# Performance work log

Hardware: AMD Instinct MI355X
Metric: run time of the kernel (lower is better)

Reference implementation:

```python
import jax, jax.numpy as jnp
import numpy as np

# Tree / encoder dims (see shape_source): root + 4 middle + 16 leaves
T_DATA = 100000
T_V = 100
WIN = 2 * T_V - 1          # (T_V-1)*2 + 1 = 199, first MLP in_dim
HID = 256                  # hid_dim
N_MID = 4                  # numel(in_idx_list[0])  (middle-level latents)
N_LEAF = 16                # numel(out_idx_list[-1]) (leaf-level latents)


def setup_inputs() -> dict:
    key = jax.random.key(0)
    ks = jax.random.split(key, 6)
    sc = lambda k, shape, fan: jax.random.normal(k, shape, jnp.float32) * (1.0 / np.sqrt(fan))
    return {
        "V_in": jax.random.normal(ks[0], (T_DATA,), jnp.float32),
        "W1": sc(ks[1], (WIN, HID), WIN),
        "b1": jnp.zeros((HID,), jnp.float32),
        "W2": sc(ks[2], (HID, N_MID), HID),
        "b2": jnp.zeros((N_MID,), jnp.float32),
        # leaf_encoder = MLP(HID, HID, N_LEAF)
        "Wl1": sc(ks[3], (HID, HID), HID),
        "bl1": jnp.zeros((HID,), jnp.float32),
        "Wl2": sc(ks[4], (HID, N_LEAF), HID),
        "bl2": jnp.zeros((N_LEAF,), jnp.float32),
    }


def reference(V_in, W1, b1, W2, b2, Wl1, bl1, Wl2, bl2):
    """Vectorized LVAE_shGLM.Encoder: the original loops over every timestep t,
    slicing pad_V_in[t:t+2*T_V-1] and running MLP.encode chains per step.
    Here all T windows are processed as one batched GEMM chain.
    MLP.encode(x) = (h = relu(x@W1+b1), mu = h@W2+b2)."""
    T = V_in.shape[0]
    pad = jnp.zeros((T + 2 * (T_V - 1),), V_in.dtype).at[T_V - 1:T_V - 1 + T].set(V_in)
    idx = jnp.arange(T)[:, None] + jnp.arange(WIN)[None, :]
    windows = pad[idx]
    # middle encoder (level 0 of the dendritic tree)
    h_mid = jax.nn.relu(windows @ W1 + b1)          # [T, HID]
    mu_mid = h_mid @ W2 + b2                        # [T, N_MID]
    # leaf encoder consumes the middle hidden state
    h_leaf = jax.nn.relu(h_mid @ Wl1 + bl1)         # [T, HID]
    mu_leaf = h_leaf @ Wl2 + bl2                    # [T, N_LEAF]
    # up_mu_array[t] = [middle mus (count 0..N_MID), leaf mus (N_MID..sub_no-1)]
    return jnp.concatenate([mu_mid, mu_leaf], axis=1)  # [T, sub_no-1] = [T, 20]
```

## Files before the change

### kernel.cpp

```cpp
#include <hip/hip_runtime.h>


typedef __bf16 bf16;
typedef __bf16 bf16x8 __attribute__((ext_vector_type(8)));
typedef __bf16 bf16x4 __attribute__((ext_vector_type(4)));
typedef float  f32x4  __attribute__((ext_vector_type(4)));
typedef float  f32x16 __attribute__((ext_vector_type(16)));

constexpr int T_DATA = 100000;
constexpr int T_V    = 100;
constexpr int WIN    = 199;
constexpr int HID    = 256;
constexpr int BT     = 128;
constexpr int CSTR   = 264;
constexpr int VLEN   = 352;
constexpr int VSTR   = 360;

constexpr int PWL1_OFF = 104 * 512;
constexpr int PW2_OFF  = 232 * 512;
constexpr int PWL2_OFF = 240 * 512;

__global__ void pack_weights(const float* __restrict__ W1, const float* __restrict__ W2,
                             const float* __restrict__ Wl1, const float* __restrict__ Wl2,
                             bf16* __restrict__ ws) {
  const int gid  = blockIdx.x * blockDim.x + threadIdx.x;
  const int lane = gid & 63;
  const int grp  = gid >> 6;
  bf16x8 v;
  if (grp < 104) {
    const int kt = grp >> 3, nt = grp & 7, n = nt * 32 + (lane & 31);
#pragma unroll
    for (int j = 0; j < 8; ++j) {
      const int k = kt * 16 + (lane >> 5) * 8 + j;
      v[j] = (k < WIN) ? (bf16)W1[k * HID + n] : (bf16)0.0f;
    }
  } else if (grp < 232) {
    const int q = grp - 104;
    const int kt = q >> 3, nt = q & 7, n = nt * 32 + (lane & 31);
#pragma unroll
    for (int j = 0; j < 8; ++j) {
      const int k = kt * 16 + (lane >> 5) * 8 + j;
      v[j] = (bf16)Wl1[k * HID + n];
    }
  } else if (grp < 240) {
    const int kt = grp - 232, m = lane & 15;
#pragma unroll
    for (int j = 0; j < 8; ++j) {
      const int k = kt * 32 + (lane >> 4) * 8 + j;
      v[j] = (m < 4) ? (bf16)W2[k * 4 + m] : (bf16)0.0f;
    }
  } else {
    const int kt = grp - 240, m = lane & 15;
#pragma unroll
    for (int j = 0; j < 8; ++j) {
      const int k = kt * 32 + (lane >> 4) * 8 + j;
      v[j] = (bf16)Wl2[k * 16 + m];
    }
  }
  *reinterpret_cast<bf16x8*>(ws + (size_t)gid * 8) = v;
}

__global__ __launch_bounds__(512, 4) void fused_enc(
    const float* __restrict__ V, const float* __restrict__ b1,
    const float* __restrict__ b2, const float* __restrict__ bl1,
    const float* __restrict__ bl2, const bf16* __restrict__ ws,
    float* __restrict__ out) {
  __shared__ bf16 Vdup[8][VSTR];
  __shared__ bf16 hbuf[BT * CSTR];

  const int tid  = threadIdx.x;
  const int lane = tid & 63;
  const int w    = tid >> 6;
  const int c5   = lane & 31;
  const int hi   = lane >> 5;
  const int m    = lane & 15;
  const int g    = lane >> 4;
  const long t0  = (long)blockIdx.x * BT;

  for (int c = tid; c < 8 * VLEN; c += 512) {
    const int p = c / VLEN, q = c - p * VLEN;
    const long src = t0 + q + p - (T_V - 1);
    const float v = (src >= 0 && src < T_DATA) ? V[src] : 0.0f;
    Vdup[p][q] = (bf16)v;
  }
  __syncthreads();

  const int p  = lane & 7;
  const int qb = (c5 + hi * 8) - p;
  const bf16* vrow = &Vdup[p][0];

  f32x16 acc[4];
#pragma unroll
  for (int nt = 0; nt < 4; ++nt) acc[nt] = (f32x16){};

#pragma unroll
  for (int kt = 0; kt < 13; ++kt) {
    const bf16x8 a = *reinterpret_cast<const bf16x8*>(
        ws + (size_t)(kt * 8 + w) * 512 + lane * 8);
#pragma unroll
    for (int nt = 0; nt < 4; ++nt) {
      const bf16x8 b = *reinterpret_cast<const bf16x8*>(vrow + qb + nt * 32 + kt * 16);
      acc[nt] = __builtin_amdgcn_mfma_f32_32x32x16_bf16(a, b, acc[nt], 0, 0, 0);
    }
  }

  {
    f32x4 bb[4];
#pragma unroll
    for (int q = 0; q < 4; ++q)
      bb[q] = *reinterpret_cast<const f32x4*>(&b1[w * 32 + 8 * q + 4 * hi]);
#pragma unroll
    for (int nt = 0; nt < 4; ++nt) {
      const int t = nt * 32 + c5;
#pragma unroll
      for (int q = 0; q < 4; ++q) {
        bf16x4 hv;
#pragma unroll
        for (int i = 0; i < 4; ++i)
          hv[i] = (bf16)fmaxf(acc[nt][4 * q + i] + bb[q][i], 0.0f);
        *reinterpret_cast<bf16x4*>(&hbuf[t * CSTR + w * 32 + 8 * q + 4 * hi]) = hv;
      }
    }
  }
  __syncthreads();

#pragma unroll
  for (int nt = 0; nt < 4; ++nt) acc[nt] = (f32x16){};
#pragma unroll
  for (int kt = 0; kt < 16; ++kt) {
    const bf16x8 a = *reinterpret_cast<const bf16x8*>(
        ws + PWL1_OFF + (size_t)(kt * 8 + w) * 512 + lane * 8);
    const int koff = kt * 16 + hi * 8;
#pragma unroll
    for (int nt = 0; nt < 4; ++nt) {
      const bf16x8 b = *reinterpret_cast<const bf16x8*>(
          &hbuf[(nt * 32 + c5) * CSTR + koff]);
      acc[nt] = __builtin_amdgcn_mfma_f32_32x32x16_bf16(a, b, acc[nt], 0, 0, 0);
    }
  }

  f32x4 mu = {0.f, 0.f, 0.f, 0.f};
#pragma unroll
  for (int kt = 0; kt < 8; ++kt) {
    const bf16x8 a = *reinterpret_cast<const bf16x8*>(
        ws + PW2_OFF + (size_t)kt * 512 + lane * 8);
    const bf16x8 b = *reinterpret_cast<const bf16x8*>(
        &hbuf[(w * 16 + m) * CSTR + kt * 32 + g * 8]);
    mu = __builtin_amdgcn_mfma_f32_16x16x32_bf16(a, b, mu, 0, 0, 0);
  }
  {
    const long t = t0 + w * 16 + m;
    if (g == 0 && t < T_DATA) {
      const f32x4 b2v = *reinterpret_cast<const f32x4*>(b2);
      f32x4 o;
#pragma unroll
      for (int j = 0; j < 4; ++j) o[j] = mu[j] + b2v[j];
      *reinterpret_cast<f32x4*>(&out[t * 20]) = o;
    }
  }
  __syncthreads();

  {
    f32x4 bb[4];
#pragma unroll
    for (int q = 0; q < 4; ++q)
      bb[q] = *reinterpret_cast<const f32x4*>(&bl1[w * 32 + 8 * q + 4 * hi]);
#pragma unroll
    for (int nt = 0; nt < 4; ++nt) {
      const int t = nt * 32 + c5;
#pragma unroll
      for (int q = 0; q < 4; ++q) {
        bf16x4 hv;
#pragma unroll
        for (int i = 0; i < 4; ++i)
          hv[i] = (bf16)fmaxf(acc[nt][4 * q + i] + bb[q][i], 0.0f);
        *reinterpret_cast<bf16x4*>(&hbuf[t * CSTR + w * 32 + 8 * q + 4 * hi]) = hv;
      }
    }
  }
  __syncthreads();

  mu = (f32x4){0.f, 0.f, 0.f, 0.f};
#pragma unroll
  for (int kq = 0; kq < 8; ++kq) {
    const bf16x8 a = *reinterpret_cast<const bf16x8*>(
        ws + PWL2_OFF + (size_t)kq * 512 + lane * 8);
    const bf16x8 b = *reinterpret_cast<const bf16x8*>(
        &hbuf[(w * 16 + m) * CSTR + kq * 32 + g * 8]);
    mu = __builtin_amdgcn_mfma_f32_16x16x32_bf16(a, b, mu, 0, 0, 0);
  }
  {
    const long t = t0 + w * 16 + m;
    if (t < T_DATA) {
      const f32x4 blv = *reinterpret_cast<const f32x4*>(&bl2[g * 4]);
      f32x4 o;
#pragma unroll
      for (int j = 0; j < 4; ++j) o[j] = mu[j] + blv[j];
      *reinterpret_cast<f32x4*>(&out[t * 20 + 4 + g * 4]) = o;
    }
  }
}

extern "C" void kernel_launch(void* const* d_in, const int* in_sizes, int n_in,
                              void* d_out, int out_size, void* d_ws, size_t ws_size,
                              hipStream_t stream) {
  const float* V   = (const float*)d_in[0];
  const float* W1  = (const float*)d_in[1];
  const float* b1  = (const float*)d_in[2];
  const float* W2  = (const float*)d_in[3];
  const float* b2  = (const float*)d_in[4];
  const float* Wl1 = (const float*)d_in[5];
  const float* bl1 = (const float*)d_in[6];
  const float* Wl2 = (const float*)d_in[7];
  const float* bl2 = (const float*)d_in[8];
  bf16* ws = (bf16*)d_ws;
  float* out = (float*)d_out;

  pack_weights<<<62, 256, 0, stream>>>(W1, W2, Wl1, Wl2, ws);

  const int grid = (T_DATA + BT - 1) / BT;
  fused_enc<<<grid, 512, 0, stream>>>(V, b1, b2, bl1, bl2, ws, out);
}
```

Before: 40.21 us.

## Split token tile into two halves and software-pipeline the MLP stages

The 128-timestep block is split into two 64-row halves with separate LDS hidden buffers. The second half's first-layer GEMM is interleaved with the first half's leaf GEMM, and the small output GEMMs are divided across warps 0-3 and 4-7 so they run concurrently. The aim is to keep the matrix cores busy across stage boundaries and shrink the per-stage accumulator footprint. The cost is extra barriers, duplicated bias loads and more complex control flow. The LDS footprint stays about the same.

```diff
diff --git a/kernel.cpp b/kernel.cpp
--- a/kernel.cpp
+++ b/kernel.cpp
@@ -66,7 +66,8 @@
     const float* __restrict__ bl2, const bf16* __restrict__ ws,
     float* __restrict__ out) {
   __shared__ bf16 Vdup[8][VSTR];
-  __shared__ bf16 hbuf[BT * CSTR];
+  __shared__ bf16 hbufA[64 * CSTR];
+  __shared__ bf16 hbufB[64 * CSTR];
 
   const int tid  = threadIdx.x;
   const int lane = tid & 63;
@@ -89,18 +90,18 @@
   const int qb = (c5 + hi * 8) - p;
   const bf16* vrow = &Vdup[p][0];
 
-  f32x16 acc[4];
-#pragma unroll
-  for (int nt = 0; nt < 4; ++nt) acc[nt] = (f32x16){};
+  f32x16 accP[2], accQ[2];
+#pragma unroll
+  for (int nt = 0; nt < 2; ++nt) { accP[nt] = (f32x16){}; }
 
 #pragma unroll
   for (int kt = 0; kt < 13; ++kt) {
     const bf16x8 a = *reinterpret_cast<const bf16x8*>(
         ws + (size_t)(kt * 8 + w) * 512 + lane * 8);
 #pragma unroll
-    for (int nt = 0; nt < 4; ++nt) {
+    for (int nt = 0; nt < 2; ++nt) {
       const bf16x8 b = *reinterpret_cast<const bf16x8*>(vrow + qb + nt * 32 + kt * 16);
-      acc[nt] = __builtin_amdgcn_mfma_f32_32x32x16_bf16(a, b, acc[nt], 0, 0, 0);
+      accP[nt] = __builtin_amdgcn_mfma_f32_32x32x16_bf16(a, b, accP[nt], 0, 0, 0);
     }
   }
 
@@ -110,45 +111,61 @@
     for (int q = 0; q < 4; ++q)
       bb[q] = *reinterpret_cast<const f32x4*>(&b1[w * 32 + 8 * q + 4 * hi]);
 #pragma unroll
-    for (int nt = 0; nt < 4; ++nt) {
+    for (int nt = 0; nt < 2; ++nt) {
       const int t = nt * 32 + c5;
 #pragma unroll
       for (int q = 0; q < 4; ++q) {
         bf16x4 hv;
 #pragma unroll
         for (int i = 0; i < 4; ++i)
-          hv[i] = (bf16)fmaxf(acc[nt][4 * q + i] + bb[q][i], 0.0f);
-        *reinterpret_cast<bf16x4*>(&hbuf[t * CSTR + w * 32 + 8 * q + 4 * hi]) = hv;
+          hv[i] = (bf16)fmaxf(accP[nt][4 * q + i] + bb[q][i], 0.0f);
+        *reinterpret_cast<bf16x4*>(&hbufA[t * CSTR + w * 32 + 8 * q + 4 * hi]) = hv;
       }
     }
   }
   __syncthreads();
 
 #pragma unroll
-  for (int nt = 0; nt < 4; ++nt) acc[nt] = (f32x16){};
-#pragma unroll
-  for (int kt = 0; kt < 16; ++kt) {
-    const bf16x8 a = *reinterpret_cast<const bf16x8*>(
+  for (int nt = 0; nt < 2; ++nt) { accP[nt] = (f32x16){}; accQ[nt] = (f32x16){}; }
+#pragma unroll 2
+  for (int kt = 0; kt < 13; ++kt) {
+    const bf16x8 a3 = *reinterpret_cast<const bf16x8*>(
+        ws + PWL1_OFF + (size_t)(kt * 8 + w) * 512 + lane * 8);
+    const bf16x8 a1 = *reinterpret_cast<const bf16x8*>(
+        ws + (size_t)(kt * 8 + w) * 512 + lane * 8);
+    const int koff = kt * 16 + hi * 8;
+#pragma unroll
+    for (int nt = 0; nt < 2; ++nt) {
+      const bf16x8 b3 = *reinterpret_cast<const bf16x8*>(
+          &hbufA[(nt * 32 + c5) * CSTR + koff]);
+      accQ[nt] = __builtin_amdgcn_mfma_f32_32x32x16_bf16(a3, b3, accQ[nt], 0, 0, 0);
+      const bf16x8 b1f = *reinterpret_cast<const bf16x8*>(
+          vrow + qb + 64 + nt * 32 + kt * 16);
+      accP[nt] = __builtin_amdgcn_mfma_f32_32x32x16_bf16(a1, b1f, accP[nt], 0, 0, 0);
+    }
+  }
+#pragma unroll
+  for (int kt = 13; kt < 16; ++kt) {
+    const bf16x8 a3 = *reinterpret_cast<const bf16x8*>(
         ws + PWL1_OFF + (size_t)(kt * 8 + w) * 512 + lane * 8);
     const int koff = kt * 16 + hi * 8;
 #pragma unroll
-    for (int nt = 0; nt < 4; ++nt) {
+    for (int nt = 0; nt < 2; ++nt) {
+      const bf16x8 b3 = *reinterpret_cast<const bf16x8*>(
+          &hbufA[(nt * 32 + c5) * CSTR + koff]);
+      accQ[nt] = __builtin_amdgcn_mfma_f32_32x32x16_bf16(a3, b3, accQ[nt], 0, 0, 0);
+    }
+  }
+  if (w < 4) {
+    f32x4 mu = {0.f, 0.f, 0.f, 0.f};
+#pragma unroll
+    for (int kt = 0; kt < 8; ++kt) {
+      const bf16x8 a = *reinterpret_cast<const bf16x8*>(
+          ws + PW2_OFF + (size_t)kt * 512 + lane * 8);
       const bf16x8 b = *reinterpret_cast<const bf16x8*>(
-          &hbuf[(nt * 32 + c5) * CSTR + koff]);
-      acc[nt] = __builtin_amdgcn_mfma_f32_32x32x16_bf16(a, b, acc[nt], 0, 0, 0);
-    }
-  }
-
-  f32x4 mu = {0.f, 0.f, 0.f, 0.f};
-#pragma unroll
-  for (int kt = 0; kt < 8; ++kt) {
-    const bf16x8 a = *reinterpret_cast<const bf16x8*>(
-        ws + PW2_OFF + (size_t)kt * 512 + lane * 8);
-    const bf16x8 b = *reinterpret_cast<const bf16x8*>(
-        &hbuf[(w * 16 + m) * CSTR + kt * 32 + g * 8]);
-    mu = __builtin_amdgcn_mfma_f32_16x16x32_bf16(a, b, mu, 0, 0, 0);
-  }
-  {
+          &hbufA[(w * 16 + m) * CSTR + kt * 32 + g * 8]);
+      mu = __builtin_amdgcn_mfma_f32_16x16x32_bf16(a, b, mu, 0, 0, 0);
+    }
     const long t = t0 + w * 16 + m;
     if (g == 0 && t < T_DATA) {
       const f32x4 b2v = *reinterpret_cast<const f32x4*>(b2);
@@ -161,36 +178,114 @@
   __syncthreads();
 
   {
+    f32x4 bbL[4], bbM[4];
+#pragma unroll
+    for (int q = 0; q < 4; ++q) {
+      bbL[q] = *reinterpret_cast<const f32x4*>(&bl1[w * 32 + 8 * q + 4 * hi]);
+      bbM[q] = *reinterpret_cast<const f32x4*>(&b1[w * 32 + 8 * q + 4 * hi]);
+    }
+#pragma unroll
+    for (int nt = 0; nt < 2; ++nt) {
+      const int t = nt * 32 + c5;
+#pragma unroll
+      for (int q = 0; q < 4; ++q) {
+        bf16x4 hvL, hvM;
+#pragma unroll
+        for (int i = 0; i < 4; ++i) {
+          hvL[i] = (bf16)fmaxf(accQ[nt][4 * q + i] + bbL[q][i], 0.0f);
+          hvM[i] = (bf16)fmaxf(accP[nt][4 * q + i] + bbM[q][i], 0.0f);
+        }
+        *reinterpret_cast<bf16x4*>(&hbufA[t * CSTR + w * 32 + 8 * q + 4 * hi]) = hvL;
+        *reinterpret_cast<bf16x4*>(&hbufB[t * CSTR + w * 32 + 8 * q + 4 * hi]) = hvM;
+      }
+    }
+  }
+  __syncthreads();
+
+#pragma unroll
+  for (int nt = 0; nt < 2; ++nt) accQ[nt] = (f32x16){};
+#pragma unroll 2
+  for (int kt = 0; kt < 16; ++kt) {
+    const bf16x8 a3 = *reinterpret_cast<const bf16x8*>(
+        ws + PWL1_OFF + (size_t)(kt * 8 + w) * 512 + lane * 8);
+    const int koff = kt * 16 + hi * 8;
+#pragma unroll
+    for (int nt = 0; nt < 2; ++nt) {
+      const bf16x8 b3 = *reinterpret_cast<const bf16x8*>(
+          &hbufB[(nt * 32 + c5) * CSTR + koff]);
+      accQ[nt] = __builtin_amdgcn_mfma_f32_32x32x16_bf16(a3, b3, accQ[nt], 0, 0, 0);
+    }
+  }
+  if (w < 4) {
+    f32x4 mu = {0.f, 0.f, 0.f, 0.f};
+#pragma unroll
+    for (int kt = 0; kt < 8; ++kt) {
+      const bf16x8 a = *reinterpret_cast<const bf16x8*>(
+          ws + PW2_OFF + (size_t)kt * 512 + lane * 8);
+      const bf16x8 b = *reinterpret_cast<const bf16x8*>(
+          &hbufB[(w * 16 + m) * CSTR + kt * 32 + g * 8]);
+      mu = __builtin_amdgcn_mfma_f32_16x16x32_bf16(a, b, mu, 0, 0, 0);
+    }
+    const long t = t0 + 64 + w * 16 + m;
+    if (g == 0 && t < T_DATA) {
+      const f32x4 b2v = *reinterpret_cast<const f32x4*>(b2);
+      f32x4 o;
+#pragma unroll
+      for (int j = 0; j < 4; ++j) o[j] = mu[j] + b2v[j];
+      *reinterpret_cast<f32x4*>(&out[t * 20]) = o;
+    }
+  } else {
+    f32x4 mu = {0.f, 0.f, 0.f, 0.f};
+#pragma unroll
+    for (int kq = 0; kq < 8; ++kq) {
+      const bf16x8 a = *reinterpret_cast<const bf16x8*>(
+          ws + PWL2_OFF + (size_t)kq * 512 + lane * 8);
+      const bf16x8 b = *reinterpret_cast<const bf16x8*>(
+          &hbufA[((w - 4) * 16 + m) * CSTR + kq * 32 + g * 8]);
+      mu = __builtin_amdgcn_mfma_f32_16x16x32_bf16(a, b, mu, 0, 0, 0);
+    }
+    const long t = t0 + (w - 4) * 16 + m;
+    if (t < T_DATA) {
+      const f32x4 blv = *reinterpret_cast<const f32x4*>(&bl2[g * 4]);
+      f32x4 o;
+#pragma unroll
+      for (int j = 0; j < 4; ++j) o[j] = mu[j] + blv[j];
+      *reinterpret_cast<f32x4*>(&out[t * 20 + 4 + g * 4]) = o;
+    }
+  }
+  __syncthreads();
+
+  {
     f32x4 bb[4];
 #pragma unroll
     for (int q = 0; q < 4; ++q)
       bb[q] = *reinterpret_cast<const f32x4*>(&bl1[w * 32 + 8 * q + 4 * hi]);
 #pragma unroll
-    for (int nt = 0; nt < 4; ++nt) {
+    for (int nt = 0; nt < 2; ++nt) {
       const int t = nt * 32 + c5;
 #pragma unroll
       for (int q = 0; q < 4; ++q) {
         bf16x4 hv;
 #pragma unroll
         for (int i = 0; i < 4; ++i)
-          hv[i] = (bf16)fmaxf(acc[nt][4 * q + i] + bb[q][i], 0.0f);
-        *reinterpret_cast<bf16x4*>(&hbuf[t * CSTR + w * 32 + 8 * q + 4 * hi]) = hv;
+          hv[i] = (bf16)fmaxf(accQ[nt][4 * q + i] + bb[q][i], 0.0f);
+        *reinterpret_cast<bf16x4*>(&hbufB[t * CSTR + w * 32 + 8 * q + 4 * hi]) = hv;
       }
     }
   }
   __syncthreads();
 
-  mu = (f32x4){0.f, 0.f, 0.f, 0.f};
-#pragma unroll
-  for (int kq = 0; kq < 8; ++kq) {
-    const bf16x8 a = *reinterpret_cast<const bf16x8*>(
-        ws + PWL2_OFF + (size_t)kq * 512 + lane * 8);
-    const bf16x8 b = *reinterpret_cast<const bf16x8*>(
-        &hbuf[(w * 16 + m) * CSTR + kq * 32 + g * 8]);
-    mu = __builtin_amdgcn_mfma_f32_16x16x32_bf16(a, b, mu, 0, 0, 0);
-  }
-  {
-    const long t = t0 + w * 16 + m;
+  if (w >= 4) {
+    f32x4 mu = {0.f, 0.f, 0.f, 0.f};
+#pragma unroll
+    for (int kq = 0; kq < 8; ++kq) {
+      const bf16x8 a = *reinterpret_cast<const bf16x8*>(
+          ws + PWL2_OFF + (size_t)kq * 512 + lane * 8);
+      const bf16x8 b = *reinterpret_cast<const bf16x8*>(
+          &hbufB[((w - 4) * 16 + m) * CSTR + kq * 32 + g * 8]);
+      mu = __builtin_amdgcn_mfma_f32_16x16x32_bf16(a, b, mu, 0, 0, 0);
+    }
+    const long t = t0 + 64 + (w - 4) * 16 + m;
     if (t < T_DATA) {
       const f32x4 blv = *reinterpret_cast<const f32x4*>(&bl2[g * 4]);
       f32x4 o;
```

Result: slower. 47.69 us (+18.6%).

## Make encoder kernel persistent over two tiles with double-buffered input windows

Applied to the files above, without the earlier changes.

Launches a fixed grid of 512 blocks, each handling up to two 128-timestep tiles, instead of one block per tile. The input window for the second tile is prefetched into a second LDS buffer during the first tile's leaf-layer work. The weight-pack launch changes from 62x256 to 248x64 threads, the same total thread count. The aim is to reduce the ragged tail of the 782-block grid and hide the V load latency, at the cost of less parallelism per tile and some extra barriers and LDS use.

```diff
diff --git a/kernel.cpp b/kernel.cpp
--- a/kernel.cpp
+++ b/kernel.cpp
@@ -15,6 +15,8 @@
 constexpr int CSTR   = 264;
 constexpr int VLEN   = 352;
 constexpr int VSTR   = 360;
+constexpr int NTILE  = 782;
+constexpr int GRID   = 512;
 
 constexpr int PWL1_OFF = 104 * 512;
 constexpr int PW2_OFF  = 232 * 512;
@@ -65,7 +67,7 @@
     const float* __restrict__ b2, const float* __restrict__ bl1,
     const float* __restrict__ bl2, const bf16* __restrict__ ws,
     float* __restrict__ out) {
-  __shared__ bf16 Vdup[8][VSTR];
+  __shared__ bf16 Vdup[2][8][VSTR];
   __shared__ bf16 hbuf[BT * CSTR];
 
   const int tid  = threadIdx.x;
@@ -75,129 +77,148 @@
   const int hi   = lane >> 5;
   const int m    = lane & 15;
   const int g    = lane >> 4;
-  const long t0  = (long)blockIdx.x * BT;
+  const int bid  = blockIdx.x;
 
   for (int c = tid; c < 8 * VLEN; c += 512) {
-    const int p = c / VLEN, q = c - p * VLEN;
-    const long src = t0 + q + p - (T_V - 1);
+    const int pp = c / VLEN, q = c - pp * VLEN;
+    const long src = (long)bid * BT + q + pp - (T_V - 1);
     const float v = (src >= 0 && src < T_DATA) ? V[src] : 0.0f;
-    Vdup[p][q] = (bf16)v;
+    Vdup[0][pp][q] = (bf16)v;
   }
   __syncthreads();
 
   const int p  = lane & 7;
   const int qb = (c5 + hi * 8) - p;
-  const bf16* vrow = &Vdup[p][0];
-
-  f32x16 acc[4];
-#pragma unroll
-  for (int nt = 0; nt < 4; ++nt) acc[nt] = (f32x16){};
-
-#pragma unroll
-  for (int kt = 0; kt < 13; ++kt) {
-    const bf16x8 a = *reinterpret_cast<const bf16x8*>(
-        ws + (size_t)(kt * 8 + w) * 512 + lane * 8);
-#pragma unroll
-    for (int nt = 0; nt < 4; ++nt) {
-      const bf16x8 b = *reinterpret_cast<const bf16x8*>(vrow + qb + nt * 32 + kt * 16);
-      acc[nt] = __builtin_amdgcn_mfma_f32_32x32x16_bf16(a, b, acc[nt], 0, 0, 0);
-    }
-  }
-
-  {
-    f32x4 bb[4];
-#pragma unroll
-    for (int q = 0; q < 4; ++q)
-      bb[q] = *reinterpret_cast<const f32x4*>(&b1[w * 32 + 8 * q + 4 * hi]);
-#pragma unroll
-    for (int nt = 0; nt < 4; ++nt) {
-      const int t = nt * 32 + c5;
-#pragma unroll
-      for (int q = 0; q < 4; ++q) {
-        bf16x4 hv;
-#pragma unroll
-        for (int i = 0; i < 4; ++i)
-          hv[i] = (bf16)fmaxf(acc[nt][4 * q + i] + bb[q][i], 0.0f);
-        *reinterpret_cast<bf16x4*>(&hbuf[t * CSTR + w * 32 + 8 * q + 4 * hi]) = hv;
-      }
-    }
-  }
-  __syncthreads();
-
-#pragma unroll
-  for (int nt = 0; nt < 4; ++nt) acc[nt] = (f32x16){};
-#pragma unroll
-  for (int kt = 0; kt < 16; ++kt) {
-    const bf16x8 a = *reinterpret_cast<const bf16x8*>(
-        ws + PWL1_OFF + (size_t)(kt * 8 + w) * 512 + lane * 8);
-    const int koff = kt * 16 + hi * 8;
-#pragma unroll
-    for (int nt = 0; nt < 4; ++nt) {
-      const bf16x8 b = *reinterpret_cast<const bf16x8*>(
-          &hbuf[(nt * 32 + c5) * CSTR + koff]);
-      acc[nt] = __builtin_amdgcn_mfma_f32_32x32x16_bf16(a, b, acc[nt], 0, 0, 0);
-    }
-  }
-
-  f32x4 mu = {0.f, 0.f, 0.f, 0.f};
-#pragma unroll
-  for (int kt = 0; kt < 8; ++kt) {
-    const bf16x8 a = *reinterpret_cast<const bf16x8*>(
-        ws + PW2_OFF + (size_t)kt * 512 + lane * 8);
-    const bf16x8 b = *reinterpret_cast<const bf16x8*>(
-        &hbuf[(w * 16 + m) * CSTR + kt * 32 + g * 8]);
-    mu = __builtin_amdgcn_mfma_f32_16x16x32_bf16(a, b, mu, 0, 0, 0);
-  }
-  {
-    const long t = t0 + w * 16 + m;
-    if (g == 0 && t < T_DATA) {
-      const f32x4 b2v = *reinterpret_cast<const f32x4*>(b2);
-      f32x4 o;
-#pragma unroll
-      for (int j = 0; j < 4; ++j) o[j] = mu[j] + b2v[j];
-      *reinterpret_cast<f32x4*>(&out[t * 20]) = o;
-    }
-  }
-  __syncthreads();
-
-  {
-    f32x4 bb[4];
-#pragma unroll
-    for (int q = 0; q < 4; ++q)
-      bb[q] = *reinterpret_cast<const f32x4*>(&bl1[w * 32 + 8 * q + 4 * hi]);
-#pragma unroll
-    for (int nt = 0; nt < 4; ++nt) {
-      const int t = nt * 32 + c5;
-#pragma unroll
-      for (int q = 0; q < 4; ++q) {
-        bf16x4 hv;
-#pragma unroll
-        for (int i = 0; i < 4; ++i)
-          hv[i] = (bf16)fmaxf(acc[nt][4 * q + i] + bb[q][i], 0.0f);
-        *reinterpret_cast<bf16x4*>(&hbuf[t * CSTR + w * 32 + 8 * q + 4 * hi]) = hv;
-      }
-    }
-  }
-  __syncthreads();
-
-  mu = (f32x4){0.f, 0.f, 0.f, 0.f};
-#pragma unroll
-  for (int kq = 0; kq < 8; ++kq) {
-    const bf16x8 a = *reinterpret_cast<const bf16x8*>(
-        ws + PWL2_OFF + (size_t)kq * 512 + lane * 8);
-    const bf16x8 b = *reinterpret_cast<const bf16x8*>(
-        &hbuf[(w * 16 + m) * CSTR + kq * 32 + g * 8]);
-    mu = __builtin_amdgcn_mfma_f32_16x16x32_bf16(a, b, mu, 0, 0, 0);
-  }
-  {
-    const long t = t0 + w * 16 + m;
-    if (t < T_DATA) {
-      const f32x4 blv = *reinterpret_cast<const f32x4*>(&bl2[g * 4]);
-      f32x4 o;
-#pragma unroll
-      for (int j = 0; j < 4; ++j) o[j] = mu[j] + blv[j];
-      *reinterpret_cast<f32x4*>(&out[t * 20 + 4 + g * 4]) = o;
-    }
+
+  const int ntiles = (bid + GRID < NTILE) ? 2 : 1;
+  int cur = 0;
+
+  for (int it = 0; it < ntiles; ++it) {
+    const long t0 = ((long)bid + (long)it * GRID) * BT;
+    const bf16* vrow = &Vdup[cur][p][0];
+
+    f32x16 acc[4];
+#pragma unroll
+    for (int nt = 0; nt < 4; ++nt) acc[nt] = (f32x16){};
+
+#pragma unroll
+    for (int kt = 0; kt < 13; ++kt) {
+      const bf16x8 a = *reinterpret_cast<const bf16x8*>(
+          ws + (size_t)(kt * 8 + w) * 512 + lane * 8);
+#pragma unroll
+      for (int nt = 0; nt < 4; ++nt) {
+        const bf16x8 b = *reinterpret_cast<const bf16x8*>(vrow + qb + nt * 32 + kt * 16);
+        acc[nt] = __builtin_amdgcn_mfma_f32_32x32x16_bf16(a, b, acc[nt], 0, 0, 0);
+      }
+    }
+
+    {
+      f32x4 bb[4];
+#pragma unroll
+      for (int q = 0; q < 4; ++q)
+        bb[q] = *reinterpret_cast<const f32x4*>(&b1[w * 32 + 8 * q + 4 * hi]);
+#pragma unroll
+      for (int nt = 0; nt < 4; ++nt) {
+        const int t = nt * 32 + c5;
+#pragma unroll
+        for (int q = 0; q < 4; ++q) {
+          bf16x4 hv;
+#pragma unroll
+          for (int i = 0; i < 4; ++i)
+            hv[i] = (bf16)fmaxf(acc[nt][4 * q + i] + bb[q][i], 0.0f);
+          *reinterpret_cast<bf16x4*>(&hbuf[t * CSTR + w * 32 + 8 * q + 4 * hi]) = hv;
+        }
+      }
+    }
+    __syncthreads();
+
+#pragma unroll
+    for (int nt = 0; nt < 4; ++nt) acc[nt] = (f32x16){};
+#pragma unroll
+    for (int kt = 0; kt < 16; ++kt) {
+      const bf16x8 a = *reinterpret_cast<const bf16x8*>(
+          ws + PWL1_OFF + (size_t)(kt * 8 + w) * 512 + lane * 8);
+      const int koff = kt * 16 + hi * 8;
+#pragma unroll
+      for (int nt = 0; nt < 4; ++nt) {
+        const bf16x8 b = *reinterpret_cast<const bf16x8*>(
+            &hbuf[(nt * 32 + c5) * CSTR + koff]);
+        acc[nt] = __builtin_amdgcn_mfma_f32_32x32x16_bf16(a, b, acc[nt], 0, 0, 0);
+      }
+    }
+
+    {
+      f32x4 mu = {0.f, 0.f, 0.f, 0.f};
+#pragma unroll
+      for (int kt = 0; kt < 8; ++kt) {
+        const bf16x8 a = *reinterpret_cast<const bf16x8*>(
+            ws + PW2_OFF + (size_t)kt * 512 + lane * 8);
+        const bf16x8 b = *reinterpret_cast<const bf16x8*>(
+            &hbuf[(w * 16 + m) * CSTR + kt * 32 + g * 8]);
+        mu = __builtin_amdgcn_mfma_f32_16x16x32_bf16(a, b, mu, 0, 0, 0);
+      }
+      const long t = t0 + w * 16 + m;
+      if (g == 0 && t < T_DATA) {
+        const f32x4 b2v = *reinterpret_cast<const f32x4*>(b2);
+        f32x4 o;
+#pragma unroll
+        for (int j = 0; j < 4; ++j) o[j] = mu[j] + b2v[j];
+        *reinterpret_cast<f32x4*>(&out[t * 20]) = o;
+      }
+    }
+
+    if (it + 1 < ntiles) {
+      for (int c = tid; c < 8 * VLEN; c += 512) {
+        const int pp = c / VLEN, q = c - pp * VLEN;
+        const long src = (long)(bid + GRID) * BT + q + pp - (T_V - 1);
+        const float v = (src >= 0 && src < T_DATA) ? V[src] : 0.0f;
+        Vdup[cur ^ 1][pp][q] = (bf16)v;
+      }
+    }
+    __syncthreads();
+
+    {
+      f32x4 bb[4];
+#pragma unroll
+      for (int q = 0; q < 4; ++q)
+        bb[q] = *reinterpret_cast<const f32x4*>(&bl1[w * 32 + 8 * q + 4 * hi]);
+#pragma unroll
+      for (int nt = 0; nt < 4; ++nt) {
+        const int t = nt * 32 + c5;
+#pragma unroll
+        for (int q = 0; q < 4; ++q) {
+          bf16x4 hv;
+#pragma unroll
+          for (int i = 0; i < 4; ++i)
+            hv[i] = (bf16)fmaxf(acc[nt][4 * q + i] + bb[q][i], 0.0f);
+          *reinterpret_cast<bf16x4*>(&hbuf[t * CSTR + w * 32 + 8 * q + 4 * hi]) = hv;
+        }
+      }
+    }
+    __syncthreads();
+
+    {
+      f32x4 mu = {0.f, 0.f, 0.f, 0.f};
+#pragma unroll
+      for (int kq = 0; kq < 8; ++kq) {
+        const bf16x8 a = *reinterpret_cast<const bf16x8*>(
+            ws + PWL2_OFF + (size_t)kq * 512 + lane * 8);
+        const bf16x8 b = *reinterpret_cast<const bf16x8*>(
+            &hbuf[(w * 16 + m) * CSTR + kq * 32 + g * 8]);
+        mu = __builtin_amdgcn_mfma_f32_16x16x32_bf16(a, b, mu, 0, 0, 0);
+      }
+      const long t = t0 + w * 16 + m;
+      if (t < T_DATA) {
+        const f32x4 blv = *reinterpret_cast<const f32x4*>(&bl2[g * 4]);
+        f32x4 o;
+#pragma unroll
+        for (int j = 0; j < 4; ++j) o[j] = mu[j] + blv[j];
+        *reinterpret_cast<f32x4*>(&out[t * 20 + 4 + g * 4]) = o;
+      }
+    }
+
+    if (it + 1 < ntiles) __syncthreads();
+    cur ^= 1;
   }
 }
 
@@ -216,8 +237,7 @@
   bf16* ws = (bf16*)d_ws;
   float* out = (float*)d_out;
 
-  pack_weights<<<62, 256, 0, stream>>>(W1, W2, Wl1, Wl2, ws);
-
-  const int grid = (T_DATA + BT - 1) / BT;
-  fused_enc<<<grid, 512, 0, stream>>>(V, b1, b2, bl1, bl2, ws, out);
+  pack_weights<<<248, 64, 0, stream>>>(W1, W2, Wl1, Wl2, ws);
+
+  fused_enc<<<GRID, 512, 0, stream>>>(V, b1, b2, bl1, bl2, ws, out);
 }
```

New measurement: 137.2 us. +241.2%, slower.
